# Kernel optimization log

Hardware: AMD Instinct MI355X
Metric: run time of the kernel (lower is better)

Reference implementation:

```python
import jax, jax.numpy as jnp
import numpy as np
from jax import lax

L, H = 16384, 1024
EPS = 1e-5


def _ln(x, w, b):
    m = jnp.mean(x, axis=-1, keepdims=True)
    v = jnp.var(x, axis=-1, keepdims=True)
    return (x - m) * lax.rsqrt(v + EPS) * w + b


def setup_inputs() -> dict:
    key = jax.random.key(0)
    ks = jax.random.split(key, 12)
    s = 0.02
    return {
        "x": jax.random.normal(ks[0], (L, H), dtype=jnp.float32),
        "ln1_w": jnp.ones((H,), jnp.float32),
        "ln1_b": jnp.zeros((H,), jnp.float32),
        "W_in": jax.random.normal(ks[1], (H, H), jnp.float32) * s,
        "b_in": jnp.zeros((H,), jnp.float32),
        "W_gate": jax.random.normal(ks[2], (H, H), jnp.float32) * s,
        "b_gate": jnp.zeros((H,), jnp.float32),
        "W_out": jax.random.normal(ks[3], (H, H), jnp.float32) * s,
        "b_out": jnp.zeros((H,), jnp.float32),
        "state_decay": jnp.zeros((H,), jnp.float32),
        "ln2_w": jnp.ones((H,), jnp.float32),
        "ln2_b": jnp.zeros((H,), jnp.float32),
        "W_ff1": jax.random.normal(ks[4], (H, 2 * H), jnp.float32) * s,
        "b_ff1": jnp.zeros((2 * H,), jnp.float32),
        "W_ff2": jax.random.normal(ks[5], (2 * H, H), jnp.float32) * s,
        "b_ff2": jnp.zeros((H,), jnp.float32),
    }


def reference(x, ln1_w, ln1_b, W_in, b_in, W_gate, b_gate, W_out, b_out,
              state_decay, ln2_w, ln2_b, W_ff1, b_ff1, W_ff2, b_ff2):
    hidden = _ln(x, ln1_w, ln1_b)                       # [L,H]
    u = hidden @ W_in + b_in                            # [L,H]
    gate = jax.nn.sigmoid(hidden @ W_gate + b_gate)     # [L,H]
    decay = jax.nn.sigmoid(state_decay)                 # [H]

    def step(s, u_t):
        s = decay * s + u_t
        return s, s

    z = jnp.zeros((x.shape[1],), x.dtype)
    _, states_f = lax.scan(step, z, u)                  # forward recurrence
    _, states_b = lax.scan(step, z, u, reverse=True)    # backward recurrence
    state_out = 0.5 * (states_f + states_b) * gate

    x = x + state_out @ W_out + b_out
    h = _ln(x, ln2_w, ln2_b)
    x = x + jax.nn.silu(h @ W_ff1 + b_ff1) @ W_ff2 + b_ff2
    return x
```

## Files before the change

### kernel.cpp

```cpp
#include <hip/hip_runtime.h>
#include <hip/hip_bf16.h>
#include <hip/hip_fp16.h>

#define L_SEQ 16384
#define HDIM  1024
#define CH    32
#define NC    (L_SEQ / CH)

typedef _Float16 f16;
typedef _Float16 f16x8 __attribute__((ext_vector_type(8)));
typedef _Float16 f16x4 __attribute__((ext_vector_type(4)));
typedef float    f32x4 __attribute__((ext_vector_type(4)));

#define AS1(p) (const __attribute__((address_space(1))) void*)(p)
#define AS3(p) (__attribute__((address_space(3))) void*)(p)

__global__ __launch_bounds__(256) void wcvt_t(const float* __restrict__ in,
                                              f16* __restrict__ out, int K, int N) {
  __shared__ float tile[32][33];
  int n0 = blockIdx.x * 32, k0 = blockIdx.y * 32;
  int tx = threadIdx.x, ty = threadIdx.y;
#pragma unroll
  for (int i = 0; i < 4; i++) {
    int k = k0 + ty + i * 8;
    tile[ty + i * 8][tx] = in[(size_t)k * N + n0 + tx];
  }
  __syncthreads();
#pragma unroll
  for (int i = 0; i < 4; i++) {
    int n = n0 + ty + i * 8;
    out[(size_t)n * K + k0 + tx] = (f16)tile[tx][ty + i * 8];
  }
}

__global__ __launch_bounds__(256) void ln_k(const float* __restrict__ x,
                                            const float* __restrict__ w,
                                            const float* __restrict__ b,
                                            f16* __restrict__ out) {
  int row = blockIdx.x;
  int t = threadIdx.x;
  const float4* xr = (const float4*)(x + (size_t)row * HDIM);
  float4 v = xr[t];
  float s  = v.x + v.y + v.z + v.w;
  float s2 = v.x * v.x + v.y * v.y + v.z * v.z + v.w * v.w;
#pragma unroll
  for (int off = 32; off > 0; off >>= 1) {
    s  += __shfl_down(s, off);
    s2 += __shfl_down(s2, off);
  }
  __shared__ float red[8];
  int wid = t >> 6, lane = t & 63;
  if (lane == 0) { red[wid] = s; red[4 + wid] = s2; }
  __syncthreads();
  if (t == 0) {
    red[0] = red[0] + red[1] + red[2] + red[3];
    red[4] = red[4] + red[5] + red[6] + red[7];
  }
  __syncthreads();
  float mean = red[0] * (1.0f / HDIM);
  float var  = red[4] * (1.0f / HDIM) - mean * mean;
  float rstd = rsqrtf(var + 1e-5f);
  float4 ww = ((const float4*)w)[t];
  float4 bb = ((const float4*)b)[t];
  f16x4 o;
  o[0] = (f16)((v.x - mean) * rstd * ww.x + bb.x);
  o[1] = (f16)((v.y - mean) * rstd * ww.y + bb.y);
  o[2] = (f16)((v.z - mean) * rstd * ww.z + bb.z);
  o[3] = (f16)((v.w - mean) * rstd * ww.w + bb.w);
  ((f16x4*)(out + (size_t)row * HDIM))[t] = o;
}

template <int ACT, int RESID, int OUTF16>
__global__ __launch_bounds__(256, 3) void gemm_bt(const f16* __restrict__ A,
                                                  const f16* __restrict__ BT,
                                                  const float* __restrict__ bias,
                                                  const float* __restrict__ resid,
                                                  void* __restrict__ Cout,
                                                  int M, int N, int K) {
  __shared__ __align__(16) f16 As[128 * 32];
  __shared__ __align__(16) f16 Bs[128 * 32];
  const int tid  = threadIdx.x;
  const int lane = tid & 63, wid = tid >> 6;
  const int wm = wid >> 1, wn = wid & 1;
  const int quad = lane >> 4, l16 = lane & 15;
  const long m0 = (long)blockIdx.y * 128;
  const long n0 = (long)blockIdx.x * 128;

  f32x4 zero = {0.f, 0.f, 0.f, 0.f};
  f32x4 acc[4][4];
#pragma unroll
  for (int i = 0; i < 4; i++)
#pragma unroll
    for (int j = 0; j < 4; j++) acc[i][j] = zero;

  for (int k0 = 0; k0 < K; k0 += 32) {
#pragma unroll
    for (int it = 0; it < 2; ++it) {
      int wboff = it * 4096 + wid * 1024;
      int eoff  = (wboff + lane * 16) >> 1;
      int r = eoff >> 5, c = eoff & 31;
      const f16* gA = A  + (m0 + r) * K + k0 + c;
      const f16* gB = BT + (n0 + r) * K + k0 + c;
      __builtin_amdgcn_global_load_lds(AS1(gA), AS3((char*)As + wboff), 16, 0, 0);
      __builtin_amdgcn_global_load_lds(AS1(gB), AS3((char*)Bs + wboff), 16, 0, 0);
    }
    __syncthreads();
    f16x8 af[4], bfr[4];
#pragma unroll
    for (int mi = 0; mi < 4; ++mi)
      af[mi] = *(const f16x8*)(As + (wm * 64 + mi * 16 + l16) * 32 + quad * 8);
#pragma unroll
    for (int ni = 0; ni < 4; ++ni)
      bfr[ni] = *(const f16x8*)(Bs + (wn * 64 + ni * 16 + l16) * 32 + quad * 8);
#pragma unroll
    for (int mi = 0; mi < 4; ++mi)
#pragma unroll
      for (int ni = 0; ni < 4; ++ni)
        acc[mi][ni] = __builtin_amdgcn_mfma_f32_16x16x32_f16(af[mi], bfr[ni], acc[mi][ni], 0, 0, 0);
    __syncthreads();
  }
#pragma unroll
  for (int mi = 0; mi < 4; ++mi) {
#pragma unroll
    for (int ni = 0; ni < 4; ++ni) {
      const long col = n0 + wn * 64 + ni * 16 + l16;
      const float bc = bias[col];
#pragma unroll
      for (int r = 0; r < 4; ++r) {
        const long row = m0 + wm * 64 + mi * 16 + quad * 4 + r;
        float v = acc[mi][ni][r] + bc;
        if (ACT == 1) v = 1.f / (1.f + __expf(-v));
        if (ACT == 2) v = v / (1.f + __expf(-v));
        if (RESID) v += resid[row * N + col];
        if (OUTF16) ((f16*)Cout)[row * N + col] = (f16)v;
        else        ((float*)Cout)[row * N + col] = v;
      }
    }
  }
}

__global__ __launch_bounds__(256) void scan_p1(const f16* __restrict__ u,
                                               const float* __restrict__ sdecay,
                                               float* __restrict__ carry_f,
                                               float* __restrict__ carry_b) {
  int tid = blockIdx.x * 256 + threadIdx.x;
  int h = tid & (HDIM - 1);
  int c = tid >> 10;
  float d = 1.f / (1.f + expf(-sdecay[h]));
  const f16* up = u + (size_t)c * CH * HDIM + h;
  float sf = 0.f, sb = 0.f, p = 1.f;
#pragma unroll
  for (int i = 0; i < CH; i++) {
    float uu = (float)up[i * HDIM];
    sf = d * sf + uu;
    sb += p * uu;
    p *= d;
  }
  carry_f[(size_t)c * HDIM + h] = sf;
  carry_b[(size_t)c * HDIM + h] = sb;
}

__global__ __launch_bounds__(256) void scan_p2(const float* __restrict__ sdecay,
                                               const float* __restrict__ carry_f,
                                               const float* __restrict__ carry_b,
                                               float* __restrict__ cin_f,
                                               float* __restrict__ cin_b) {
  int tid = blockIdx.x * 256 + threadIdx.x;
  int h = tid & (HDIM - 1);
  int dir = tid >> 10;
  float d = 1.f / (1.f + expf(-sdecay[h]));
  float dT = powf(d, (float)CH);
  float S = 0.f;
  if (dir == 0) {
#pragma unroll 4
    for (int c = 0; c < NC; c++) {
      cin_f[(size_t)c * HDIM + h] = S;
      S = dT * S + carry_f[(size_t)c * HDIM + h];
    }
  } else {
#pragma unroll 4
    for (int c = NC - 1; c >= 0; c--) {
      cin_b[(size_t)c * HDIM + h] = S;
      S = dT * S + carry_b[(size_t)c * HDIM + h];
    }
  }
}

__global__ __launch_bounds__(256) void scan_p3(const f16* __restrict__ u,
                                               const f16* __restrict__ gate,
                                               const float* __restrict__ sdecay,
                                               const float* __restrict__ cin_f,
                                               const float* __restrict__ cin_b,
                                               f16* __restrict__ state_out) {
  int tid = blockIdx.x * 256 + threadIdx.x;
  int h = tid & (HDIM - 1);
  int c = tid >> 10;
  float d = 1.f / (1.f + expf(-sdecay[h]));
  const f16* up = u    + (size_t)c * CH * HDIM + h;
  const f16* gp = gate + (size_t)c * CH * HDIM + h;
  f16* op = state_out  + (size_t)c * CH * HDIM + h;
  float ur[CH], sf[CH];
#pragma unroll
  for (int i = 0; i < CH; i++) ur[i] = (float)up[i * HDIM];
  float s = cin_f[(size_t)c * HDIM + h];
#pragma unroll
  for (int i = 0; i < CH; i++) { s = d * s + ur[i]; sf[i] = s; }
  s = cin_b[(size_t)c * HDIM + h];
#pragma unroll
  for (int i = CH - 1; i >= 0; i--) {
    s = d * s + ur[i];
    float g = (float)gp[i * HDIM];
    op[i * HDIM] = (f16)(0.5f * (sf[i] + s) * g);
  }
}

extern "C" void kernel_launch(void* const* d_in, const int* in_sizes, int n_in,
                              void* d_out, int out_size, void* d_ws, size_t ws_size,
                              hipStream_t stream) {
  const float* x      = (const float*)d_in[0];
  const float* ln1_w  = (const float*)d_in[1];
  const float* ln1_b  = (const float*)d_in[2];
  const float* W_in   = (const float*)d_in[3];
  const float* b_in   = (const float*)d_in[4];
  const float* W_gate = (const float*)d_in[5];
  const float* b_gate = (const float*)d_in[6];
  const float* W_out  = (const float*)d_in[7];
  const float* b_out  = (const float*)d_in[8];
  const float* sdecay = (const float*)d_in[9];
  const float* ln2_w  = (const float*)d_in[10];
  const float* ln2_b  = (const float*)d_in[11];
  const float* W_ff1  = (const float*)d_in[12];
  const float* b_ff1  = (const float*)d_in[13];
  const float* W_ff2  = (const float*)d_in[14];
  const float* b_ff2  = (const float*)d_in[15];
  float* out = (float*)d_out;

  char* ws = (char*)d_ws;
  const size_t MB32 = 33554432, MB64 = 67108864;
  f16*   hidden  = (f16*)(ws);
  f16*   u       = (f16*)(ws + MB32);
  f16*   gate    = (f16*)(ws + 2 * MB32);
  float* x2      = (float*)(ws + 3 * MB32);
  f16*   ff      = (f16*)(ws + 3 * MB32 + MB64);
  char*  wbase   = ws + 3 * MB32 + 2 * MB64;
  f16* wt_in   = (f16*)(wbase);
  f16* wt_gate = (f16*)(wbase + 2097152);
  f16* wt_out  = (f16*)(wbase + 2 * 2097152);
  f16* wt_ff1  = (f16*)(wbase + 3 * 2097152);
  f16* wt_ff2  = (f16*)(wbase + 3 * 2097152 + 4194304);
  char* cbase  = wbase + 3 * 2097152 + 2 * 4194304;
  float* carry_f = (float*)(cbase);
  float* carry_b = (float*)(cbase + 2097152);
  float* cin_f   = (float*)(cbase + 2 * 2097152);
  float* cin_b   = (float*)(cbase + 3 * 2097152);
  f16* state_out = hidden;
  f16* h2        = u;

  dim3 tb(32, 8);
  wcvt_t<<<dim3(32, 32), tb, 0, stream>>>(W_in,   wt_in,   1024, 1024);
  wcvt_t<<<dim3(32, 32), tb, 0, stream>>>(W_gate, wt_gate, 1024, 1024);
  wcvt_t<<<dim3(32, 32), tb, 0, stream>>>(W_out,  wt_out,  1024, 1024);
  wcvt_t<<<dim3(64, 32), tb, 0, stream>>>(W_ff1,  wt_ff1,  1024, 2048);
  wcvt_t<<<dim3(32, 64), tb, 0, stream>>>(W_ff2,  wt_ff2,  2048, 1024);

  ln_k<<<L_SEQ, 256, 0, stream>>>(x, ln1_w, ln1_b, hidden);

  gemm_bt<0, 0, 1><<<dim3(8, 128), 256, 0, stream>>>(hidden, wt_in,   b_in,   nullptr, u,    L_SEQ, 1024, 1024);
  gemm_bt<1, 0, 1><<<dim3(8, 128), 256, 0, stream>>>(hidden, wt_gate, b_gate, nullptr, gate, L_SEQ, 1024, 1024);

  scan_p1<<<2048, 256, 0, stream>>>(u, sdecay, carry_f, carry_b);
  scan_p2<<<8, 256, 0, stream>>>(sdecay, carry_f, carry_b, cin_f, cin_b);
  scan_p3<<<2048, 256, 0, stream>>>(u, gate, sdecay, cin_f, cin_b, state_out);

  gemm_bt<0, 1, 0><<<dim3(8, 128), 256, 0, stream>>>(state_out, wt_out, b_out, x, x2, L_SEQ, 1024, 1024);

  ln_k<<<L_SEQ, 256, 0, stream>>>(x2, ln2_w, ln2_b, h2);

  gemm_bt<2, 0, 1><<<dim3(16, 128), 256, 0, stream>>>(h2, wt_ff1, b_ff1, nullptr, ff,  L_SEQ, 2048, 1024);
  gemm_bt<0, 1, 0><<<dim3(8, 128),  256, 0, stream>>>(ff, wt_ff2, b_ff2, x2,      out, L_SEQ, 1024, 2048);
}
```

Baseline: 655.9 us.

## Fuse in/gate GEMMs, store residuals in fp16, and remap GEMM blocks per XCD

```diff
diff --git a/kernel.cpp b/kernel.cpp
--- a/kernel.cpp
+++ b/kernel.cpp
@@ -36,7 +36,8 @@
 __global__ __launch_bounds__(256) void ln_k(const float* __restrict__ x,
                                             const float* __restrict__ w,
                                             const float* __restrict__ b,
-                                            f16* __restrict__ out) {
+                                            f16* __restrict__ out,
+                                            f16* __restrict__ xcopy) {
   int row = blockIdx.x;
   int t = threadIdx.x;
   const float4* xr = (const float4*)(x + (size_t)row * HDIM);
@@ -68,14 +69,58 @@
   o[2] = (f16)((v.z - mean) * rstd * ww.z + bb.z);
   o[3] = (f16)((v.w - mean) * rstd * ww.w + bb.w);
   ((f16x4*)(out + (size_t)row * HDIM))[t] = o;
-}
-
-template <int ACT, int RESID, int OUTF16>
+  if (xcopy) {
+    f16x4 c;
+    c[0] = (f16)v.x; c[1] = (f16)v.y; c[2] = (f16)v.z; c[3] = (f16)v.w;
+    ((f16x4*)(xcopy + (size_t)row * HDIM))[t] = c;
+  }
+}
+
+__global__ __launch_bounds__(256) void ln_k16(const f16* __restrict__ x,
+                                              const float* __restrict__ w,
+                                              const float* __restrict__ b,
+                                              f16* __restrict__ out) {
+  int row = blockIdx.x;
+  int t = threadIdx.x;
+  f16x4 xv = ((const f16x4*)(x + (size_t)row * HDIM))[t];
+  float4 v = {(float)xv[0], (float)xv[1], (float)xv[2], (float)xv[3]};
+  float s  = v.x + v.y + v.z + v.w;
+  float s2 = v.x * v.x + v.y * v.y + v.z * v.z + v.w * v.w;
+#pragma unroll
+  for (int off = 32; off > 0; off >>= 1) {
+    s  += __shfl_down(s, off);
+    s2 += __shfl_down(s2, off);
+  }
+  __shared__ float red[8];
+  int wid = t >> 6, lane = t & 63;
+  if (lane == 0) { red[wid] = s; red[4 + wid] = s2; }
+  __syncthreads();
+  if (t == 0) {
+    red[0] = red[0] + red[1] + red[2] + red[3];
+    red[4] = red[4] + red[5] + red[6] + red[7];
+  }
+  __syncthreads();
+  float mean = red[0] * (1.0f / HDIM);
+  float var  = red[4] * (1.0f / HDIM) - mean * mean;
+  float rstd = rsqrtf(var + 1e-5f);
+  float4 ww = ((const float4*)w)[t];
+  float4 bb = ((const float4*)b)[t];
+  f16x4 o;
+  o[0] = (f16)((v.x - mean) * rstd * ww.x + bb.x);
+  o[1] = (f16)((v.y - mean) * rstd * ww.y + bb.y);
+  o[2] = (f16)((v.z - mean) * rstd * ww.z + bb.z);
+  o[3] = (f16)((v.w - mean) * rstd * ww.w + bb.w);
+  ((f16x4*)(out + (size_t)row * HDIM))[t] = o;
+}
+
+template <int MODE, int RESID, int OUTF16>
 __global__ __launch_bounds__(256, 3) void gemm_bt(const f16* __restrict__ A,
                                                   const f16* __restrict__ BT,
                                                   const float* __restrict__ bias,
-                                                  const float* __restrict__ resid,
+                                                  const float* __restrict__ bias2,
+                                                  const f16* __restrict__ resid,
                                                   void* __restrict__ Cout,
+                                                  void* __restrict__ Cout2,
                                                   int M, int N, int K) {
   __shared__ __align__(16) f16 As[128 * 32];
   __shared__ __align__(16) f16 Bs[128 * 32];
@@ -83,15 +128,22 @@
   const int lane = tid & 63, wid = tid >> 6;
   const int wm = wid >> 1, wn = wid & 1;
   const int quad = lane >> 4, l16 = lane & 15;
-  const long m0 = (long)blockIdx.y * 128;
-  const long n0 = (long)blockIdx.x * 128;
+
+  const int nbx = N >> 7, nby = M >> 7;
+  const int b = blockIdx.x;
+  const int xcd = b & 7;
+  const int i = b >> 3;
+  const int strips = nby >> 3;
+  const int rs = i / nbx, cb = i - rs * nbx;
+  const long m0 = (long)(xcd * strips + rs) << 7;
+  const long n0 = (long)cb << 7;
 
   f32x4 zero = {0.f, 0.f, 0.f, 0.f};
   f32x4 acc[4][4];
 #pragma unroll
-  for (int i = 0; i < 4; i++)
-#pragma unroll
-    for (int j = 0; j < 4; j++) acc[i][j] = zero;
+  for (int i2 = 0; i2 < 4; i2++)
+#pragma unroll
+    for (int j = 0; j < 4; j++) acc[i2][j] = zero;
 
   for (int k0 = 0; k0 < K; k0 += 32) {
 #pragma unroll
@@ -124,16 +176,26 @@
 #pragma unroll
     for (int ni = 0; ni < 4; ++ni) {
       const long col = n0 + wn * 64 + ni * 16 + l16;
-      const float bc = bias[col];
+      float bc;
+      if (MODE == 3) bc = (col < HDIM) ? bias[col] : bias2[col - HDIM];
+      else           bc = bias[col];
 #pragma unroll
       for (int r = 0; r < 4; ++r) {
         const long row = m0 + wm * 64 + mi * 16 + quad * 4 + r;
         float v = acc[mi][ni][r] + bc;
-        if (ACT == 1) v = 1.f / (1.f + __expf(-v));
-        if (ACT == 2) v = v / (1.f + __expf(-v));
-        if (RESID) v += resid[row * N + col];
-        if (OUTF16) ((f16*)Cout)[row * N + col] = (f16)v;
-        else        ((float*)Cout)[row * N + col] = v;
+        if (MODE == 2) v = v / (1.f + __expf(-v));
+        if (MODE == 3) {
+          if (col < HDIM) {
+            ((f16*)Cout)[row * HDIM + col] = (f16)v;
+          } else {
+            float g = 1.f / (1.f + __expf(-v));
+            ((f16*)Cout2)[row * HDIM + (col - HDIM)] = (f16)g;
+          }
+        } else {
+          if (RESID) v += (float)resid[row * N + col];
+          if (OUTF16) ((f16*)Cout)[row * N + col] = (f16)v;
+          else        ((float*)Cout)[row * N + col] = v;
+        }
       }
     }
   }
@@ -237,18 +299,18 @@
 
   char* ws = (char*)d_ws;
   const size_t MB32 = 33554432, MB64 = 67108864;
-  f16*   hidden  = (f16*)(ws);
-  f16*   u       = (f16*)(ws + MB32);
-  f16*   gate    = (f16*)(ws + 2 * MB32);
-  float* x2      = (float*)(ws + 3 * MB32);
-  f16*   ff      = (f16*)(ws + 3 * MB32 + MB64);
-  char*  wbase   = ws + 3 * MB32 + 2 * MB64;
-  f16* wt_in   = (f16*)(wbase);
-  f16* wt_gate = (f16*)(wbase + 2097152);
-  f16* wt_out  = (f16*)(wbase + 2 * 2097152);
-  f16* wt_ff1  = (f16*)(wbase + 3 * 2097152);
-  f16* wt_ff2  = (f16*)(wbase + 3 * 2097152 + 4194304);
-  char* cbase  = wbase + 3 * 2097152 + 2 * 4194304;
+  f16* hidden = (f16*)(ws);
+  f16* xh     = (f16*)(ws + MB32);
+  f16* u      = (f16*)(ws + 2 * MB32);
+  f16* gate   = (f16*)(ws + 3 * MB32);
+  f16* x2h    = (f16*)(ws + 4 * MB32);
+  f16* ff     = (f16*)(ws + 5 * MB32);
+  char* wbase = ws + 5 * MB32 + MB64;
+  f16* wt_ug  = (f16*)(wbase);
+  f16* wt_out = (f16*)(wbase + 4194304);
+  f16* wt_ff1 = (f16*)(wbase + 4194304 + 2097152);
+  f16* wt_ff2 = (f16*)(wbase + 2 * 4194304 + 2097152);
+  char* cbase = wbase + 3 * 4194304 + 2097152;
   float* carry_f = (float*)(cbase);
   float* carry_b = (float*)(cbase + 2097152);
   float* cin_f   = (float*)(cbase + 2 * 2097152);
@@ -257,25 +319,29 @@
   f16* h2        = u;
 
   dim3 tb(32, 8);
-  wcvt_t<<<dim3(32, 32), tb, 0, stream>>>(W_in,   wt_in,   1024, 1024);
-  wcvt_t<<<dim3(32, 32), tb, 0, stream>>>(W_gate, wt_gate, 1024, 1024);
-  wcvt_t<<<dim3(32, 32), tb, 0, stream>>>(W_out,  wt_out,  1024, 1024);
-  wcvt_t<<<dim3(64, 32), tb, 0, stream>>>(W_ff1,  wt_ff1,  1024, 2048);
-  wcvt_t<<<dim3(32, 64), tb, 0, stream>>>(W_ff2,  wt_ff2,  2048, 1024);
-
-  ln_k<<<L_SEQ, 256, 0, stream>>>(x, ln1_w, ln1_b, hidden);
-
-  gemm_bt<0, 0, 1><<<dim3(8, 128), 256, 0, stream>>>(hidden, wt_in,   b_in,   nullptr, u,    L_SEQ, 1024, 1024);
-  gemm_bt<1, 0, 1><<<dim3(8, 128), 256, 0, stream>>>(hidden, wt_gate, b_gate, nullptr, gate, L_SEQ, 1024, 1024);
+  wcvt_t<<<dim3(32, 32), tb, 0, stream>>>(W_in,   wt_ug,                 1024, 1024);
+  wcvt_t<<<dim3(32, 32), tb, 0, stream>>>(W_gate, wt_ug + 1024 * 1024,   1024, 1024);
+  wcvt_t<<<dim3(32, 32), tb, 0, stream>>>(W_out,  wt_out,                1024, 1024);
+  wcvt_t<<<dim3(64, 32), tb, 0, stream>>>(W_ff1,  wt_ff1,                1024, 2048);
+  wcvt_t<<<dim3(32, 64), tb, 0, stream>>>(W_ff2,  wt_ff2,                2048, 1024);
+
+  ln_k<<<L_SEQ, 256, 0, stream>>>(x, ln1_w, ln1_b, hidden, xh);
+
+  gemm_bt<3, 0, 1><<<2048, 256, 0, stream>>>(hidden, wt_ug, b_in, b_gate, nullptr,
+                                             u, gate, L_SEQ, 2048, 1024);
 
   scan_p1<<<2048, 256, 0, stream>>>(u, sdecay, carry_f, carry_b);
   scan_p2<<<8, 256, 0, stream>>>(sdecay, carry_f, carry_b, cin_f, cin_b);
   scan_p3<<<2048, 256, 0, stream>>>(u, gate, sdecay, cin_f, cin_b, state_out);
 
-  gemm_bt<0, 1, 0><<<dim3(8, 128), 256, 0, stream>>>(state_out, wt_out, b_out, x, x2, L_SEQ, 1024, 1024);
-
-  ln_k<<<L_SEQ, 256, 0, stream>>>(x2, ln2_w, ln2_b, h2);
-
-  gemm_bt<2, 0, 1><<<dim3(16, 128), 256, 0, stream>>>(h2, wt_ff1, b_ff1, nullptr, ff,  L_SEQ, 2048, 1024);
-  gemm_bt<0, 1, 0><<<dim3(8, 128),  256, 0, stream>>>(ff, wt_ff2, b_ff2, x2,      out, L_SEQ, 1024, 2048);
-}
+  gemm_bt<0, 1, 1><<<1024, 256, 0, stream>>>(state_out, wt_out, b_out, nullptr, xh,
+                                             x2h, nullptr, L_SEQ, 1024, 1024);
+
+  ln_k16<<<L_SEQ, 256, 0, stream>>>(x2h, ln2_w, ln2_b, h2);
+
+  gemm_bt<2, 0, 1><<<2048, 256, 0, stream>>>(h2, wt_ff1, b_ff1, nullptr, nullptr,
+                                             ff, nullptr, L_SEQ, 2048, 1024);
+
+  gemm_bt<0, 1, 0><<<1024, 256, 0, stream>>>(ff, wt_ff2, b_ff2, nullptr, x2h,
+                                             out, nullptr, L_SEQ, 1024, 2048);
+}
```

Result: faster. 600.2 us (-8.5%).
